# Performance work log

Measured on AMD Instinct MI355X. Metric: run time of the kernel, lower is better.

Reference implementation:

```python
import jax, jax.numpy as jnp
import numpy as np

TT_SHAPES = [16, 16, 16, 16, 16, 16]
TT_RANKS = [1, 64, 64, 64, 64, 64, 1]
OUT_FEATURES = 4096  # 16*16*16
IN_FEATURES = 4096   # 16*16*16
N_TOKENS = 8192


def setup_inputs() -> dict:
    key = jax.random.key(0)
    ks = jax.random.split(key, len(TT_SHAPES) + 2)
    inp = {}
    for i in range(len(TT_SHAPES)):
        shape = (TT_RANKS[i], TT_SHAPES[i], TT_RANKS[i + 1])
        # xavier-uniform-like init
        fan = TT_RANKS[i] * TT_SHAPES[i] + TT_SHAPES[i] * TT_RANKS[i + 1]
        bound = float(np.sqrt(6.0 / fan))
        inp[f"core{i}"] = jax.random.uniform(ks[i], shape, jnp.float32, -bound, bound)
    inp["x"] = jax.random.normal(ks[-2], (N_TOKENS, IN_FEATURES), dtype=jnp.float32)
    b_bound = 1.0 / np.sqrt(IN_FEATURES)
    inp["b"] = jax.random.uniform(ks[-1], (OUT_FEATURES,), jnp.float32, -b_bound, b_bound)
    return inp


def _recover_weight(cores):
    # chain of reshape+matmul contractions, exactly as TTLinearR._recover_weight
    w = cores[0]
    for i in range(1, len(cores)):
        w = w.reshape(-1, TT_RANKS[i]) @ cores[i].reshape(TT_RANKS[i], -1)
    return w.reshape(OUT_FEATURES, IN_FEATURES)


def reference(x, core0, core1, core2, core3, core4, core5, b):
    w = _recover_weight([core0, core1, core2, core3, core4, core5])
    # F.linear(x, w, b) == x @ w.T + b
    return x @ w.T + b
```

## Files before the change

### kernel.cpp

```cpp
#include <hip/hip_runtime.h>


#define TOK 8192
#define DIN 4096
#define DOUT 4096
#define RNK 64

#define TB 32
#define BK 256
#define NKI (DIN / BK)
#define XS 264
#define AS 72
#define TSTR 66

typedef __bf16 bf16x8 __attribute__((ext_vector_type(8)));
typedef float f32x4 __attribute__((ext_vector_type(4)));

__device__ __forceinline__ unsigned short f2bf(float f) {
  unsigned int u = __float_as_uint(f);
  u += 0x7FFFu + ((u >> 16) & 1u);
  return (unsigned short)(u >> 16);
}

__global__ void chain1(const float* __restrict__ c0, const float* __restrict__ c1,
                       const float* __restrict__ c4, const float* __restrict__ c5,
                       float* __restrict__ S1, float* __restrict__ S3) {
  int b = blockIdx.x;
  if (b < 64) {
    int idx = b * 256 + threadIdx.x;
    int m = idx >> 10, n = idx & 1023;
    const float* a = c0 + m * 64;
    float acc = 0.f;
#pragma unroll
    for (int k = 0; k < 64; ++k) acc += a[k] * c1[k * 1024 + n];
    S1[idx] = acc;
  } else {
    int idx = (b - 64) * 256 + threadIdx.x;
    int m = idx >> 4, n = idx & 15;
    const float* a = c4 + m * 64;
    float acc = 0.f;
#pragma unroll
    for (int k = 0; k < 64; ++k) acc += a[k] * c5[k * 16 + n];
    S3[idx] = acc;
  }
}

__global__ void chain2(const float* __restrict__ S1, const float* __restrict__ c2,
                       const float* __restrict__ c3, const float* __restrict__ S3,
                       unsigned short* __restrict__ Abf, unsigned short* __restrict__ Bbf) {
  int b = blockIdx.x;
  if (b < 1024) {
    int idx = b * 256 + threadIdx.x;
    int m = idx >> 10, n = idx & 1023;
    const float* a = S1 + m * 64;
    float acc = 0.f;
#pragma unroll
    for (int k = 0; k < 64; ++k) acc += a[k] * c2[k * 1024 + n];
    Abf[idx] = f2bf(acc);
  } else {
    int idx = (b - 1024) * 256 + threadIdx.x;
    int m = idx >> 8, n = idx & 255;
    const float* a = c3 + m * 64;
    float acc = 0.f;
#pragma unroll
    for (int k = 0; k < 64; ++k) acc += a[k] * S3[k * 256 + n];
    Bbf[idx] = f2bf(acc);
  }
}

__global__ __launch_bounds__(512)
void fused_ttl(const float* __restrict__ x, const unsigned short* __restrict__ Bbf,
               const unsigned short* __restrict__ Abf, const float* __restrict__ bias,
               float* __restrict__ out) {
  __shared__ __align__(16) unsigned short sm[39168];
  unsigned short* ts = sm;
  unsigned short* xs = sm + 2304;
  unsigned short* bs = sm + 2304 + 32 * XS;
  float* tred = (float*)(sm + 2304);
  unsigned short* as_ = sm + 2304;

  const int tid = threadIdx.x;
  const int m0 = blockIdx.x * TB;
  const int lane = tid & 63, wv = tid >> 6;
  const int r = lane & 15, q = lane >> 4;
  const int khalf = wv >> 2, jrank = wv & 3;

  int xr[4], xc[4], br[4], bc[4];
#pragma unroll
  for (int j = 0; j < 4; ++j) {
    int f = j * 512 + tid;
    xr[j] = f >> 6; xc[j] = f & 63;
    br[j] = f >> 5; bc[j] = f & 31;
  }

  float4 px[4]; uint4 pb[4];
#pragma unroll
  for (int j = 0; j < 4; ++j) {
    px[j] = *(const float4*)&x[(size_t)(m0 + xr[j]) * DIN + xc[j] * 4];
    pb[j] = *(const uint4*)&Bbf[(size_t)br[j] * DIN + bc[j] * 8];
  }

  f32x4 acc1[2];
#pragma unroll
  for (int i = 0; i < 2; ++i) acc1[i] = (f32x4){0.f, 0.f, 0.f, 0.f};

#pragma unroll 1
  for (int ki = 0; ki < NKI; ++ki) {
    __syncthreads();
#pragma unroll
    for (int j = 0; j < 4; ++j) {
      ushort4 h = {f2bf(px[j].x), f2bf(px[j].y), f2bf(px[j].z), f2bf(px[j].w)};
      *(ushort4*)&xs[xr[j] * XS + xc[j] * 4] = h;
      *(uint4*)&bs[br[j] * XS + bc[j] * 8] = pb[j];
    }
    if (ki + 1 < NKI) {
      int k0n = (ki + 1) * BK;
#pragma unroll
      for (int j = 0; j < 4; ++j) {
        px[j] = *(const float4*)&x[(size_t)(m0 + xr[j]) * DIN + k0n + xc[j] * 4];
        pb[j] = *(const uint4*)&Bbf[(size_t)br[j] * DIN + k0n + bc[j] * 8];
      }
    }
    __syncthreads();
#pragma unroll
    for (int s32 = 0; s32 < 4; ++s32) {
      const int koff = khalf * 128 + s32 * 32 + q * 8;
      bf16x8 bfr = *(const bf16x8*)&bs[(jrank * 16 + r) * XS + koff];
#pragma unroll
      for (int i = 0; i < 2; ++i) {
        bf16x8 afr = *(const bf16x8*)&xs[(i * 16 + r) * XS + koff];
        acc1[i] = __builtin_amdgcn_mfma_f32_16x16x32_bf16(afr, bfr, acc1[i], 0, 0, 0);
      }
    }
  }

  __syncthreads();
  if (wv >= 4) {
#pragma unroll
    for (int i = 0; i < 2; ++i)
#pragma unroll
      for (int g = 0; g < 4; ++g)
        tred[(i * 16 + q * 4 + g) * TSTR + jrank * 16 + r] = acc1[i][g];
  }
  __syncthreads();
  if (wv < 4) {
#pragma unroll
    for (int i = 0; i < 2; ++i)
#pragma unroll
      for (int g = 0; g < 4; ++g) {
        float v = acc1[i][g] + tred[(i * 16 + q * 4 + g) * TSTR + jrank * 16 + r];
        ts[(i * 16 + q * 4 + g) * AS + jrank * 16 + r] = f2bf(v);
      }
  }
  __syncthreads();

#pragma unroll 1
  for (int ni = 0; ni < DOUT / 512; ++ni) {
    const int n0 = ni * 512;
#pragma unroll
    for (int j = 0; j < 8; ++j) {
      int f = j * 512 + tid;
      int row = f >> 3, c = f & 7;
      *(uint4*)&as_[row * AS + c * 8] =
          *(const uint4*)&Abf[(size_t)(n0 + row) * RNK + c * 8];
    }
    __syncthreads();

    f32x4 acc2[2][4];
#pragma unroll
    for (int i = 0; i < 2; ++i)
#pragma unroll
      for (int j = 0; j < 4; ++j) acc2[i][j] = (f32x4){0.f, 0.f, 0.f, 0.f};

#pragma unroll
    for (int s32 = 0; s32 < 2; ++s32) {
      bf16x8 a2[2], b2[4];
#pragma unroll
      for (int i = 0; i < 2; ++i)
        a2[i] = *(const bf16x8*)&ts[(i * 16 + r) * AS + s32 * 32 + q * 8];
#pragma unroll
      for (int j = 0; j < 4; ++j)
        b2[j] = *(const bf16x8*)&as_[(wv * 64 + j * 16 + r) * AS + s32 * 32 + q * 8];
#pragma unroll
      for (int i = 0; i < 2; ++i)
#pragma unroll
        for (int j = 0; j < 4; ++j)
          acc2[i][j] = __builtin_amdgcn_mfma_f32_16x16x32_bf16(a2[i], b2[j], acc2[i][j], 0, 0, 0);
    }

    float bb[4];
#pragma unroll
    for (int j = 0; j < 4; ++j) bb[j] = bias[n0 + wv * 64 + j * 16 + r];

#pragma unroll
    for (int i = 0; i < 2; ++i)
#pragma unroll
      for (int g = 0; g < 4; ++g) {
        size_t rowg = (size_t)(m0 + i * 16 + q * 4 + g) * DOUT;
#pragma unroll
        for (int j = 0; j < 4; ++j)
          out[rowg + n0 + wv * 64 + j * 16 + r] = acc2[i][j][g] + bb[j];
      }
    __syncthreads();
  }
}

extern "C" void kernel_launch(void* const* d_in, const int* in_sizes, int n_in,
                              void* d_out, int out_size, void* d_ws, size_t ws_size,
                              hipStream_t stream) {
  const float* c0 = (const float*)d_in[0];
  const float* c1 = (const float*)d_in[1];
  const float* c2 = (const float*)d_in[2];
  const float* c3 = (const float*)d_in[3];
  const float* c4 = (const float*)d_in[4];
  const float* c5 = (const float*)d_in[5];
  const float* x  = (const float*)d_in[6];
  const float* bias = (const float*)d_in[7];
  float* out = (float*)d_out;

  char* ws = (char*)d_ws;
  float*          S1  = (float*)(ws);
  float*          S3  = (float*)(ws + (1u << 16));
  unsigned short* Abf = (unsigned short*)(ws + (2u << 16));
  unsigned short* Bbf = (unsigned short*)(ws + (2u << 16) + (1u << 19));

  chain1<<<128, 256, 0, stream>>>(c0, c1, c4, c5, S1, S3);
  chain2<<<2048, 256, 0, stream>>>(S1, c2, c3, S3, Abf, Bbf);
  fused_ttl<<<256, 512, 0, stream>>>(x, Bbf, Abf, bias, out);
}
```

Measured before the change: 303.6 us.

## Split fused TT-linear kernel into two GEMM kernels with more blocks

After: 324.9 us. 1.07x slower.

```diff
diff --git a/kernel.cpp b/kernel.cpp
--- a/kernel.cpp
+++ b/kernel.cpp
@@ -6,15 +6,19 @@
 #define DOUT 4096
 #define RNK 64
 
-#define TB 32
+#define TB 16
 #define BK 256
 #define NKI (DIN / BK)
 #define XS 264
+#define TSTR 66
+
+#define G2M 128
+#define G2N 256
 #define AS 72
-#define TSTR 66
 
 typedef __bf16 bf16x8 __attribute__((ext_vector_type(8)));
 typedef float f32x4 __attribute__((ext_vector_type(4)));
+typedef float f32x16 __attribute__((ext_vector_type(16)));
 
 __device__ __forceinline__ unsigned short f2bf(float f) {
   unsigned int u = __float_as_uint(f);
@@ -69,15 +73,12 @@
 }
 
 __global__ __launch_bounds__(512)
-void fused_ttl(const float* __restrict__ x, const unsigned short* __restrict__ Bbf,
-               const unsigned short* __restrict__ Abf, const float* __restrict__ bias,
-               float* __restrict__ out) {
-  __shared__ __align__(16) unsigned short sm[39168];
-  unsigned short* ts = sm;
-  unsigned short* xs = sm + 2304;
-  unsigned short* bs = sm + 2304 + 32 * XS;
-  float* tred = (float*)(sm + 2304);
-  unsigned short* as_ = sm + 2304;
+void gemm1_t(const float* __restrict__ x, const unsigned short* __restrict__ Bbf,
+             unsigned short* __restrict__ tb) {
+  __shared__ __align__(16) unsigned short sm[(TB + 64) * XS];
+  unsigned short* xs = sm;
+  unsigned short* bs = sm + TB * XS;
+  float* tred = (float*)sm;
 
   const int tid = threadIdx.x;
   const int m0 = blockIdx.x * TB;
@@ -85,123 +86,129 @@
   const int r = lane & 15, q = lane >> 4;
   const int khalf = wv >> 2, jrank = wv & 3;
 
-  int xr[4], xc[4], br[4], bc[4];
+  int xr[2], xc[2], br[4], bc[4];
+#pragma unroll
+  for (int j = 0; j < 2; ++j) {
+    int f = j * 512 + tid;
+    xr[j] = f >> 6; xc[j] = f & 63;
+  }
 #pragma unroll
   for (int j = 0; j < 4; ++j) {
     int f = j * 512 + tid;
-    xr[j] = f >> 6; xc[j] = f & 63;
     br[j] = f >> 5; bc[j] = f & 31;
   }
 
-  float4 px[4]; uint4 pb[4];
-#pragma unroll
-  for (int j = 0; j < 4; ++j) {
+  float4 px[2]; uint4 pb[4];
+#pragma unroll
+  for (int j = 0; j < 2; ++j)
     px[j] = *(const float4*)&x[(size_t)(m0 + xr[j]) * DIN + xc[j] * 4];
+#pragma unroll
+  for (int j = 0; j < 4; ++j)
     pb[j] = *(const uint4*)&Bbf[(size_t)br[j] * DIN + bc[j] * 8];
-  }
-
-  f32x4 acc1[2];
-#pragma unroll
-  for (int i = 0; i < 2; ++i) acc1[i] = (f32x4){0.f, 0.f, 0.f, 0.f};
+
+  f32x4 acc1 = (f32x4){0.f, 0.f, 0.f, 0.f};
 
 #pragma unroll 1
   for (int ki = 0; ki < NKI; ++ki) {
     __syncthreads();
 #pragma unroll
-    for (int j = 0; j < 4; ++j) {
+    for (int j = 0; j < 2; ++j) {
       ushort4 h = {f2bf(px[j].x), f2bf(px[j].y), f2bf(px[j].z), f2bf(px[j].w)};
       *(ushort4*)&xs[xr[j] * XS + xc[j] * 4] = h;
+    }
+#pragma unroll
+    for (int j = 0; j < 4; ++j)
       *(uint4*)&bs[br[j] * XS + bc[j] * 8] = pb[j];
-    }
     if (ki + 1 < NKI) {
       int k0n = (ki + 1) * BK;
 #pragma unroll
-      for (int j = 0; j < 4; ++j) {
+      for (int j = 0; j < 2; ++j)
         px[j] = *(const float4*)&x[(size_t)(m0 + xr[j]) * DIN + k0n + xc[j] * 4];
+#pragma unroll
+      for (int j = 0; j < 4; ++j)
         pb[j] = *(const uint4*)&Bbf[(size_t)br[j] * DIN + k0n + bc[j] * 8];
-      }
     }
     __syncthreads();
 #pragma unroll
     for (int s32 = 0; s32 < 4; ++s32) {
       const int koff = khalf * 128 + s32 * 32 + q * 8;
+      bf16x8 afr = *(const bf16x8*)&xs[r * XS + koff];
       bf16x8 bfr = *(const bf16x8*)&bs[(jrank * 16 + r) * XS + koff];
-#pragma unroll
-      for (int i = 0; i < 2; ++i) {
-        bf16x8 afr = *(const bf16x8*)&xs[(i * 16 + r) * XS + koff];
-        acc1[i] = __builtin_amdgcn_mfma_f32_16x16x32_bf16(afr, bfr, acc1[i], 0, 0, 0);
-      }
+      acc1 = __builtin_amdgcn_mfma_f32_16x16x32_bf16(afr, bfr, acc1, 0, 0, 0);
     }
   }
 
   __syncthreads();
   if (wv >= 4) {
 #pragma unroll
-    for (int i = 0; i < 2; ++i)
-#pragma unroll
-      for (int g = 0; g < 4; ++g)
-        tred[(i * 16 + q * 4 + g) * TSTR + jrank * 16 + r] = acc1[i][g];
+    for (int g = 0; g < 4; ++g)
+      tred[(q * 4 + g) * TSTR + jrank * 16 + r] = acc1[g];
   }
   __syncthreads();
   if (wv < 4) {
 #pragma unroll
-    for (int i = 0; i < 2; ++i)
-#pragma unroll
-      for (int g = 0; g < 4; ++g) {
-        float v = acc1[i][g] + tred[(i * 16 + q * 4 + g) * TSTR + jrank * 16 + r];
-        ts[(i * 16 + q * 4 + g) * AS + jrank * 16 + r] = f2bf(v);
-      }
+    for (int g = 0; g < 4; ++g) {
+      float v = acc1[g] + tred[(q * 4 + g) * TSTR + jrank * 16 + r];
+      tb[(size_t)(m0 + q * 4 + g) * RNK + jrank * 16 + r] = f2bf(v);
+    }
+  }
+}
+
+__global__ __launch_bounds__(512)
+void gemm2_y(const unsigned short* __restrict__ tbf, const unsigned short* __restrict__ Abf,
+             const float* __restrict__ bias, float* __restrict__ out) {
+  __shared__ __align__(16) unsigned short sm[(G2M + G2N) * AS];
+  unsigned short* ts = sm;
+  unsigned short* as_ = sm + G2M * AS;
+
+  const int tid = threadIdx.x;
+  const int m0 = blockIdx.y * G2M, n0 = blockIdx.x * G2N;
+  const int lane = tid & 63, wv = tid >> 6;
+  const int l31 = lane & 31, hi = lane >> 5;
+  const int mw = (wv >> 1) * 32, nw = (wv & 1) * 128;
+
+#pragma unroll
+  for (int j = 0; j < 2; ++j) {
+    int f = j * 512 + tid;
+    int row = f >> 3, c = f & 7;
+    *(uint4*)&ts[row * AS + c * 8] = *(const uint4*)&tbf[(size_t)(m0 + row) * RNK + c * 8];
+  }
+#pragma unroll
+  for (int j = 0; j < 4; ++j) {
+    int f = j * 512 + tid;
+    int row = f >> 3, c = f & 7;
+    *(uint4*)&as_[row * AS + c * 8] = *(const uint4*)&Abf[(size_t)(n0 + row) * RNK + c * 8];
   }
   __syncthreads();
 
-#pragma unroll 1
-  for (int ni = 0; ni < DOUT / 512; ++ni) {
-    const int n0 = ni * 512;
-#pragma unroll
-    for (int j = 0; j < 8; ++j) {
-      int f = j * 512 + tid;
-      int row = f >> 3, c = f & 7;
-      *(uint4*)&as_[row * AS + c * 8] =
-          *(const uint4*)&Abf[(size_t)(n0 + row) * RNK + c * 8];
-    }
-    __syncthreads();
-
-    f32x4 acc2[2][4];
-#pragma unroll
-    for (int i = 0; i < 2; ++i)
-#pragma unroll
-      for (int j = 0; j < 4; ++j) acc2[i][j] = (f32x4){0.f, 0.f, 0.f, 0.f};
-
-#pragma unroll
-    for (int s32 = 0; s32 < 2; ++s32) {
-      bf16x8 a2[2], b2[4];
-#pragma unroll
-      for (int i = 0; i < 2; ++i)
-        a2[i] = *(const bf16x8*)&ts[(i * 16 + r) * AS + s32 * 32 + q * 8];
-#pragma unroll
-      for (int j = 0; j < 4; ++j)
-        b2[j] = *(const bf16x8*)&as_[(wv * 64 + j * 16 + r) * AS + s32 * 32 + q * 8];
-#pragma unroll
-      for (int i = 0; i < 2; ++i)
-#pragma unroll
-        for (int j = 0; j < 4; ++j)
-          acc2[i][j] = __builtin_amdgcn_mfma_f32_16x16x32_bf16(a2[i], b2[j], acc2[i][j], 0, 0, 0);
-    }
-
-    float bb[4];
-#pragma unroll
-    for (int j = 0; j < 4; ++j) bb[j] = bias[n0 + wv * 64 + j * 16 + r];
-
-#pragma unroll
-    for (int i = 0; i < 2; ++i)
-#pragma unroll
-      for (int g = 0; g < 4; ++g) {
-        size_t rowg = (size_t)(m0 + i * 16 + q * 4 + g) * DOUT;
-#pragma unroll
-        for (int j = 0; j < 4; ++j)
-          out[rowg + n0 + wv * 64 + j * 16 + r] = acc2[i][j][g] + bb[j];
-      }
-    __syncthreads();
+  f32x16 acc[4];
+#pragma unroll
+  for (int j = 0; j < 4; ++j)
+#pragma unroll
+    for (int e = 0; e < 16; ++e) acc[j][e] = 0.f;
+
+#pragma unroll
+  for (int ks = 0; ks < 4; ++ks) {
+    bf16x8 a = *(const bf16x8*)&ts[(mw + l31) * AS + ks * 16 + hi * 8];
+#pragma unroll
+    for (int j = 0; j < 4; ++j) {
+      bf16x8 b = *(const bf16x8*)&as_[(nw + j * 32 + l31) * AS + ks * 16 + hi * 8];
+      acc[j] = __builtin_amdgcn_mfma_f32_32x32x16_bf16(a, b, acc[j], 0, 0, 0);
+    }
+  }
+
+  float bb[4];
+#pragma unroll
+  for (int j = 0; j < 4; ++j) bb[j] = bias[n0 + nw + j * 32 + l31];
+
+#pragma unroll
+  for (int j = 0; j < 4; ++j) {
+    const int col = n0 + nw + j * 32 + l31;
+#pragma unroll
+    for (int reg = 0; reg < 16; ++reg) {
+      int rowt = (reg & 3) + 8 * (reg >> 2) + 4 * hi;
+      out[(size_t)(m0 + mw + rowt) * DOUT + col] = acc[j][reg] + bb[j];
+    }
   }
 }
 
@@ -223,8 +230,10 @@
   float*          S3  = (float*)(ws + (1u << 16));
   unsigned short* Abf = (unsigned short*)(ws + (2u << 16));
   unsigned short* Bbf = (unsigned short*)(ws + (2u << 16) + (1u << 19));
+  unsigned short* tbf = (unsigned short*)(ws + (2u << 16) + (2u << 19));
 
   chain1<<<128, 256, 0, stream>>>(c0, c1, c4, c5, S1, S3);
   chain2<<<2048, 256, 0, stream>>>(S1, c2, c3, S3, Abf, Bbf);
-  fused_ttl<<<256, 512, 0, stream>>>(x, Bbf, Abf, bias, out);
-}
+  gemm1_t<<<TOK / TB, 512, 0, stream>>>(x, Bbf, tbf);
+  gemm2_y<<<dim3(DOUT / G2N, TOK / G2M), 512, 0, stream>>>(tbf, Abf, bias, out);
+}
```
